# Kernel tuning notes

Hardware: AMD Instinct MI355X
Metric: run time of the kernel (lower is better)

Reference implementation:

```python
import jax, jax.numpy as jnp
import numpy as np

NHEAD = 8; DM = 512; DFF = 2048; L = 4; S = 1024; NTOK = 51; MLP = 256; CLASSES = 7
GH = 3; GHID = 64; GCLS = 5; ALPHA = 0.2
HD = DM // NHEAD

_ADJ = np.array([[0,1,0,0,0],[1,1,1,1,0],[1,0,1,0,1],[1,0,0,1,1],[0,0,1,1,1]], dtype=np.int32)


def setup_inputs():
    key = jax.random.key(0)
    ks = jax.random.split(key, 24)
    r = lambda k, s, sc=0.05: jax.random.normal(k, s, jnp.float32) * sc
    return {
        'x': jax.random.normal(ks[0], (5, S, NTOK), jnp.float32),
        'adj': jnp.asarray(_ADJ),
        'W_enc': r(ks[1], (NTOK, DM)), 'b_enc': jnp.zeros((DM,), jnp.float32),
        'cls_tok': r(ks[2], (1, 1, DM)),
        'pos_emb': r(ks[3], (S + 1, DM)),
        'Wq': r(ks[4], (L, DM, DM)), 'bq': jnp.zeros((L, DM), jnp.float32),
        'Wk': r(ks[5], (L, DM, DM)), 'bk': jnp.zeros((L, DM), jnp.float32),
        'Wv': r(ks[6], (L, DM, DM)), 'bv': jnp.zeros((L, DM), jnp.float32),
        'Wo': r(ks[7], (L, DM, DM)), 'bo': jnp.zeros((L, DM), jnp.float32),
        'W1': r(ks[8], (L, DM, DFF)), 'b1': jnp.zeros((L, DFF), jnp.float32),
        'W2': r(ks[9], (L, DFF, DM)), 'b2': jnp.zeros((L, DM), jnp.float32),
        'g1': jnp.ones((L, DM), jnp.float32), 'be1': jnp.zeros((L, DM), jnp.float32),
        'g2': jnp.ones((L, DM), jnp.float32), 'be2': jnp.zeros((L, DM), jnp.float32),
        'Wd1': r(ks[10], (DM, MLP)), 'bd1': jnp.zeros((MLP,), jnp.float32),
        'Wd2': r(ks[11], (MLP, CLASSES)), 'bd2': jnp.zeros((CLASSES,), jnp.float32),
        'Wg': r(ks[12], (GH, 3, GHID), 0.3), 'ag': r(ks[13], (GH, 2 * GHID), 0.3),
        'Wgo': r(ks[14], (GH * GHID, GCLS), 0.3), 'ago': r(ks[15], (2 * GCLS,), 0.3),
    }


def _layernorm(x, g, b, eps=1e-5):
    m = x.mean(-1, keepdims=True)
    v = ((x - m) ** 2).mean(-1, keepdims=True)
    return (x - m) * jax.lax.rsqrt(v + eps) * g + b


def _gat_attn_layer(h_in, W, a, mask):
    # standard pyGAT GraphAttentionLayer: e_ij = LeakyReLU(a1.h_i + a2.h_j)
    F = W.shape[1]
    h = h_in @ W                                                    # [N, F]
    e = jax.nn.leaky_relu((h @ a[:F])[:, None] + (h @ a[F:])[None, :], ALPHA)
    att = jax.nn.softmax(jnp.where(mask, e, -9e15), axis=-1)        # adjacency-masked softmax
    return att @ h


def _gat(xg, mask, Wg, ag, Wgo, ago):
    # xg: [5 nodes, 3 feats]; GH attention heads concatenated, then output layer
    heads = jax.vmap(lambda W, a: jax.nn.elu(_gat_attn_layer(xg, W, a, mask)))(Wg, ag)  # [GH,5,GHID]
    hcat = jnp.transpose(heads, (1, 0, 2)).reshape(xg.shape[0], GH * GHID)
    out = jax.nn.elu(_gat_attn_layer(hcat, Wgo, ago, mask))         # [5, GCLS]
    return jax.nn.log_softmax(out, axis=1)


def _forward(x, adj, params):
    (W_enc, b_enc, cls_tok, pos_emb, Wq, bq, Wk, bk, Wv, bv, Wo, bo,
     W1, b1, W2, b2, g1, be1, g2, be2, Wd1, bd1, Wd2, bd2, Wg, ag, Wgo, ago) = params
    mask = adj > 0
    # --- batched GAT: the source loops over T timesteps x 5 feature groups; here fully vectorized ---
    # x[:, :, :15] : batch(=5 nodes) x T x 15 -> [T*5groups, 5 nodes, 3]
    xg = x[:, :, :15].reshape(5, S, 5, 3)
    xg = jnp.transpose(xg, (1, 2, 0, 3)).reshape(S * 5, 5, 3)
    gat_out = jax.vmap(lambda g: _gat(g, mask, Wg, ag, Wgo, ago))(xg)
    gat_out = gat_out.reshape(S, 5, 5, GCLS)                        # [T, group, node, class]
    # --- transformer branch (eval mode: dropout = identity) ---
    h = x @ W_enc + b_enc                                           # [5, S, DM]
    h = jnp.concatenate([jnp.broadcast_to(cls_tok, (5, 1, DM)), h], axis=1)
    h = h + pos_emb[None]
    for i in range(L):
        q = (h @ Wq[i] + bq[i]).reshape(5, S + 1, NHEAD, HD)
        k = (h @ Wk[i] + bk[i]).reshape(5, S + 1, NHEAD, HD)
        v = (h @ Wv[i] + bv[i]).reshape(5, S + 1, NHEAD, HD)
        sc = jnp.einsum('bthd,bshd->bhts', q, k) / jnp.sqrt(jnp.float32(HD))
        att = jax.nn.softmax(sc, axis=-1)
        o = jnp.einsum('bhts,bshd->bthd', att, v).reshape(5, S + 1, DM) @ Wo[i] + bo[i]
        h = _layernorm(h + o, g1[i], be1[i])
        f = jax.nn.relu(h @ W1[i] + b1[i]) @ W2[i] + b2[i]
        h = _layernorm(h + f, g2[i], be2[i])
    cls = h[:, 0, :]                                                # lambda: x[:, 0, :]
    out = (cls @ Wd1 + bd1) @ Wd2 + bd2                             # no activation between dense layers (as in source)
    return out, gat_out


def reference(x, adj, W_enc, b_enc, cls_tok, pos_emb, Wq, bq, Wk, bk, Wv, bv, Wo, bo, W1, b1, W2, b2, g1, be1, g2, be2, Wd1, bd1, Wd2, bd2, Wg, ag, Wgo, ago):
    params = (W_enc, b_enc, cls_tok, pos_emb, Wq, bq, Wk, bk, Wv, bv, Wo, bo,
              W1, b1, W2, b2, g1, be1, g2, be2, Wd1, bd1, Wd2, bd2, Wg, ag, Wgo, ago)
    return _forward(x, adj, params)
```

## Files before the change

### kernel.cpp

```cpp
#include <hip/hip_runtime.h>
#include <hip/hip_bf16.h>
#include <math.h>

#define NBATCH 5
#define SEQ    1024
#define T      1025
#define ROWS   (NBATCH * T)
#define MP     5248
#define DM     512
#define DFF    2048
#define NHEAD  8
#define HD     64
#define NTOK   51
#define MLPDIM 256
#define NCLS   7
#define GH     3
#define GHID   64
#define GCLS   5
#define NGRAPH (SEQ * 5)
#define QKVN   1536
#define TPAD   1152

typedef __attribute__((ext_vector_type(8))) short bf16x8;
typedef __attribute__((ext_vector_type(4))) float f32x4;

#define GM_AS(p)  ((const __attribute__((address_space(1))) void*)(p))
#define LDS_AS(p) ((__attribute__((address_space(3))) void*)(p))

__device__ __forceinline__ unsigned short f2bf(float f) {
    unsigned int u = __float_as_uint(f);
    unsigned int r = (u + 0x7FFFu + ((u >> 16) & 1u)) >> 16;
    return (unsigned short)r;
}
__device__ __forceinline__ float bf2f(unsigned short u) {
    return __uint_as_float((unsigned int)u << 16);
}

__global__ __launch_bounds__(256) void setup_kernel(
    const float* __restrict__ Wq, const float* __restrict__ Wk,
    const float* __restrict__ Wv, const float* __restrict__ Wo_,
    const float* __restrict__ W1, const float* __restrict__ W2,
    const float* __restrict__ bq, const float* __restrict__ bk,
    const float* __restrict__ bv,
    unsigned short* __restrict__ Wqkvt, unsigned short* __restrict__ Wot,
    unsigned short* __restrict__ W1t, unsigned short* __restrict__ W2t,
    float* __restrict__ bqkv)
{
    int id = blockIdx.x;
    if (id >= 12288) {
        int i = id - 12288;
        #pragma unroll
        for (int rep = 0; rep < 2; ++rep) {
            int t = threadIdx.x + rep * 256;
            bqkv[i * QKVN + t]        = bq[i * DM + t];
            bqkv[i * QKVN + 512 + t]  = bk[i * DM + t];
            bqkv[i * QKVN + 1024 + t] = bv[i * DM + t];
        }
        return;
    }
    const float* W; unsigned short* Wt; int K, N, z, bx, by; long dstride;
    if (id < 4096) {
        int g = id >> 10, lid = id & 1023;
        K = DM; N = DM;
        z = lid >> 8; int r2 = lid & 255; by = r2 >> 4; bx = r2 & 15;
        if (g < 3) { W = (g == 0) ? Wq : (g == 1) ? Wk : Wv;
                     Wt = Wqkvt + (size_t)g * DM * DM; dstride = (long)QKVN * DM; }
        else       { W = Wo_; Wt = Wot; dstride = (long)DM * DM; }
    } else if (id < 8192) {
        int lid = id - 4096;
        K = DM; N = DFF;
        z = lid >> 10; int r2 = lid & 1023; by = r2 >> 6; bx = r2 & 63;
        W = W1; Wt = W1t; dstride = (long)DM * DFF;
    } else {
        int lid = id - 8192;
        K = DFF; N = DM;
        z = lid >> 10; int r2 = lid & 1023; by = r2 >> 4; bx = r2 & 15;
        W = W2; Wt = W2t; dstride = (long)DFF * DM;
    }
    const float* Wm = W + (size_t)z * K * N;
    unsigned short* Wo2 = Wt + (size_t)z * dstride;
    __shared__ float tile[32][33];
    int bX = bx * 32, bY = by * 32;
    int tx = threadIdx.x & 31, ty = threadIdx.x >> 5;
    #pragma unroll
    for (int i = 0; i < 32; i += 8)
        tile[ty + i][tx] = Wm[(size_t)(bY + ty + i) * N + bX + tx];
    __syncthreads();
    #pragma unroll
    for (int i = 0; i < 32; i += 8)
        Wo2[(size_t)(bX + ty + i) * K + bY + tx] = f2bf(tile[tx][ty + i]);
}

__global__ __launch_bounds__(256) void gemm_mfma(
    const unsigned short* __restrict__ A, const unsigned short* __restrict__ Bt,
    const float* __restrict__ bias, float* __restrict__ Cf,
    unsigned short* __restrict__ Cb, int N, int K, int relu)
{
    __shared__ unsigned short As[128 * 64];
    __shared__ unsigned short Bs[128 * 64];
    int tid = threadIdx.x;
    int l = tid & 63, w = tid >> 6;
    int wr = w & 1, wc = w >> 1;
    int mlane = l & 15, quad = l >> 4;
    int m0 = blockIdx.y * 128, n0 = blockIdx.x * 128;

    f32x4 acc[4][4] = {};

    for (int k0 = 0; k0 < K; k0 += 64) {
        __syncthreads();
        #pragma unroll
        for (int it = 0; it < 4; ++it) {
            int c = tid + it * 256;
            int row = c >> 3, cc = c & 7;
            const unsigned short* ga = A  + (size_t)(m0 + row) * K + k0 + cc * 8;
            __builtin_amdgcn_global_load_lds(GM_AS(ga), LDS_AS(As + c * 8), 16, 0, 0);
            const unsigned short* gb = Bt + (size_t)(n0 + row) * K + k0 + cc * 8;
            __builtin_amdgcn_global_load_lds(GM_AS(gb), LDS_AS(Bs + c * 8), 16, 0, 0);
        }
        __syncthreads();
        #pragma unroll
        for (int half = 0; half < 2; ++half) {
            int ko = half * 32 + quad * 8;
            bf16x8 afrag[4], bfrag[4];
            #pragma unroll
            for (int mi = 0; mi < 4; ++mi)
                afrag[mi] = *(const bf16x8*)(As + (wr * 64 + mi * 16 + mlane) * 64 + ko);
            #pragma unroll
            for (int ni = 0; ni < 4; ++ni)
                bfrag[ni] = *(const bf16x8*)(Bs + (wc * 64 + ni * 16 + mlane) * 64 + ko);
            #pragma unroll
            for (int mi = 0; mi < 4; ++mi)
                #pragma unroll
                for (int ni = 0; ni < 4; ++ni)
                    acc[mi][ni] = __builtin_amdgcn_mfma_f32_16x16x32_bf16(
                        afrag[mi], bfrag[ni], acc[mi][ni], 0, 0, 0);
        }
    }

    #pragma unroll
    for (int mi = 0; mi < 4; ++mi) {
        #pragma unroll
        for (int r = 0; r < 4; ++r) {
            int gm = m0 + wr * 64 + mi * 16 + quad * 4 + r;
            size_t rowoff = (size_t)gm * N;
            #pragma unroll
            for (int ni = 0; ni < 4; ++ni) {
                int gn = n0 + wc * 64 + ni * 16 + mlane;
                float val = acc[mi][ni][r] + bias[gn];
                if (relu) val = fmaxf(val, 0.f);
                if (Cb) Cb[rowoff + gn] = f2bf(val);
                else    Cf[rowoff + gn] = val;
            }
        }
    }
}

__global__ __launch_bounds__(256) void gemm_mfma_sk(
    const unsigned short* __restrict__ A, const unsigned short* __restrict__ Bt,
    unsigned short* __restrict__ part, int N, int K)
{
    __shared__ unsigned short As[128 * 64];
    __shared__ unsigned short Bs[128 * 64];
    int tid = threadIdx.x;
    int l = tid & 63, w = tid >> 6;
    int wr = w & 1, wc = w >> 1;
    int mlane = l & 15, quad = l >> 4;
    int m0 = blockIdx.y * 128, n0 = blockIdx.x * 128;
    int kper = K / gridDim.z;
    int kbeg = blockIdx.z * kper;

    f32x4 acc[4][4] = {};

    for (int k0 = kbeg; k0 < kbeg + kper; k0 += 64) {
        __syncthreads();
        #pragma unroll
        for (int it = 0; it < 4; ++it) {
            int c = tid + it * 256;
            int row = c >> 3, cc = c & 7;
            const unsigned short* ga = A  + (size_t)(m0 + row) * K + k0 + cc * 8;
            __builtin_amdgcn_global_load_lds(GM_AS(ga), LDS_AS(As + c * 8), 16, 0, 0);
            const unsigned short* gb = Bt + (size_t)(n0 + row) * K + k0 + cc * 8;
            __builtin_amdgcn_global_load_lds(GM_AS(gb), LDS_AS(Bs + c * 8), 16, 0, 0);
        }
        __syncthreads();
        #pragma unroll
        for (int half = 0; half < 2; ++half) {
            int ko = half * 32 + quad * 8;
            bf16x8 afrag[4], bfrag[4];
            #pragma unroll
            for (int mi = 0; mi < 4; ++mi)
                afrag[mi] = *(const bf16x8*)(As + (wr * 64 + mi * 16 + mlane) * 64 + ko);
            #pragma unroll
            for (int ni = 0; ni < 4; ++ni)
                bfrag[ni] = *(const bf16x8*)(Bs + (wc * 64 + ni * 16 + mlane) * 64 + ko);
            #pragma unroll
            for (int mi = 0; mi < 4; ++mi)
                #pragma unroll
                for (int ni = 0; ni < 4; ++ni)
                    acc[mi][ni] = __builtin_amdgcn_mfma_f32_16x16x32_bf16(
                        afrag[mi], bfrag[ni], acc[mi][ni], 0, 0, 0);
        }
    }

    unsigned short* pz = part + (size_t)blockIdx.z * MP * N;
    #pragma unroll
    for (int mi = 0; mi < 4; ++mi) {
        #pragma unroll
        for (int r = 0; r < 4; ++r) {
            int gm = m0 + wr * 64 + mi * 16 + quad * 4 + r;
            size_t rowoff = (size_t)gm * N;
            #pragma unroll
            for (int ni = 0; ni < 4; ++ni) {
                int gn = n0 + wc * 64 + ni * 16 + mlane;
                pz[rowoff + gn] = f2bf(acc[mi][ni][r]);
            }
        }
    }
}

__global__ __launch_bounds__(256) void vtrans_kernel(
    const unsigned short* __restrict__ vb, unsigned short* __restrict__ vt, int qs)
{
    __shared__ unsigned short tile[64][72];
    int bh = blockIdx.y;
    int b = bh >> 3, h = bh & 7;
    int t0 = blockIdx.x * 64;
    int tid = threadIdx.x;
    #pragma unroll
    for (int it = 0; it < 2; ++it) {
        int c = tid + it * 256;
        int key = c >> 3, cc = c & 7;
        int gk = t0 + key; if (gk >= T) gk = T - 1;
        *(bf16x8*)(&tile[key][cc * 8]) =
            *(const bf16x8*)(vb + ((size_t)b * T + gk) * qs + h * HD + cc * 8);
    }
    __syncthreads();
    #pragma unroll
    for (int it = 0; it < 2; ++it) {
        int c = tid + it * 256;
        int d = c >> 3, cc = c & 7;
        unsigned short tmp[8];
        #pragma unroll
        for (int j = 0; j < 8; ++j) tmp[j] = tile[cc * 8 + j][d];
        *(bf16x8*)(vt + ((size_t)bh * 64 + d) * TPAD + t0 + cc * 8) = *(bf16x8*)tmp;
    }
}

#define AQT 64
#define NR 9
__global__ __launch_bounds__(256) void attn_mfma(
    const unsigned short* __restrict__ qb, const unsigned short* __restrict__ kb,
    const unsigned short* __restrict__ vt, unsigned short* __restrict__ ob,
    int qs)
{
    __shared__ unsigned short Ks[128 * 72];
    __shared__ unsigned short Vs[64 * 136];
    __shared__ unsigned short Ps[4][16 * 72];
    int bh = blockIdx.y;
    int b = bh >> 3, h = bh & 7;
    int t0 = blockIdx.x * AQT;
    int tid = threadIdx.x;
    int l = tid & 63, w = tid >> 6;
    int ml = l & 15, quad = l >> 4;
    size_t rowbase = (size_t)b * T;
    const unsigned short* vtb = vt + (size_t)bh * 64 * TPAD;

    int qrow = t0 + w * 16 + ml; if (qrow >= T) qrow = T - 1;
    const unsigned short* qp = qb + (rowbase + qrow) * qs + h * HD + quad * 8;
    bf16x8 qf0 = *(const bf16x8*)qp;
    bf16x8 qf1 = *(const bf16x8*)(qp + 32);

    int krow = tid >> 3, kcc = tid & 7;
    int vd   = tid >> 4, vck = tid & 15;

    f32x4 oacc[4] = {};
    float lrow[4] = {0.f, 0.f, 0.f, 0.f};

    bf16x8 kr[4], vr[4];
    #pragma unroll
    for (int i = 0; i < 4; ++i) {
        int gk = krow + i * 32; if (gk >= T) gk = T - 1;
        kr[i] = *(const bf16x8*)(kb + (rowbase + gk) * qs + h * HD + kcc * 8);
        vr[i] = *(const bf16x8*)(vtb + (size_t)(vd + i * 16) * TPAD + vck * 8);
    }

    for (int rnd = 0; rnd < NR; ++rnd) {
        int c0 = rnd * 128;
        __syncthreads();
        #pragma unroll
        for (int i = 0; i < 4; ++i) {
            *(bf16x8*)(Ks + (krow + i * 32) * 72 + kcc * 8) = kr[i];
            *(bf16x8*)(Vs + (vd + i * 16) * 136 + vck * 8) = vr[i];
        }
        __syncthreads();
        if (rnd + 1 < NR) {
            int n0k = c0 + 128;
            #pragma unroll
            for (int i = 0; i < 4; ++i) {
                int gk = n0k + krow + i * 32; if (gk >= T) gk = T - 1;
                kr[i] = *(const bf16x8*)(kb + (rowbase + gk) * qs + h * HD + kcc * 8);
                vr[i] = *(const bf16x8*)(vtb + (size_t)(vd + i * 16) * TPAD + n0k + vck * 8);
            }
        }

        #pragma unroll
        for (int p = 0; p < 2; ++p) {
            int kb0 = p * 64;
            f32x4 s[4] = {};
            #pragma unroll
            for (int ni = 0; ni < 4; ++ni) {
                const unsigned short* kfp = Ks + (kb0 + ni * 16 + ml) * 72 + quad * 8;
                bf16x8 kf0 = *(const bf16x8*)kfp;
                bf16x8 kf1 = *(const bf16x8*)(kfp + 32);
                s[ni] = __builtin_amdgcn_mfma_f32_16x16x32_bf16(qf0, kf0, s[ni], 0, 0, 0);
                s[ni] = __builtin_amdgcn_mfma_f32_16x16x32_bf16(qf1, kf1, s[ni], 0, 0, 0);
            }
            #pragma unroll
            for (int ni = 0; ni < 4; ++ni) {
                bool valid = (c0 + kb0 + ni * 16 + ml) < T;
                #pragma unroll
                for (int r = 0; r < 4; ++r) {
                    float pv = valid ? __expf(s[ni][r] * 0.125f) : 0.f;
                    s[ni][r] = pv;
                    lrow[r] += pv;
                }
            }
            unsigned short* pw = Ps[w];
            #pragma unroll
            for (int r = 0; r < 4; ++r)
                #pragma unroll
                for (int ni = 0; ni < 4; ++ni)
                    pw[(quad * 4 + r) * 72 + ((ni * 16 + ml) ^ (quad << 4))] = f2bf(s[ni][r]);
            int sw = ((ml >> 2) & 3) << 4;
            #pragma unroll
            for (int kc = 0; kc < 2; ++kc) {
                bf16x8 pf = *(const bf16x8*)(pw + ml * 72 + ((kc * 32 + quad * 8) ^ sw));
                #pragma unroll
                for (int ni = 0; ni < 4; ++ni) {
                    bf16x8 vf = *(const bf16x8*)(Vs + (ni * 16 + ml) * 136 + kb0 + kc * 32 + quad * 8);
                    oacc[ni] = __builtin_amdgcn_mfma_f32_16x16x32_bf16(pf, vf, oacc[ni], 0, 0, 0);
                }
            }
        }
    }

    #pragma unroll
    for (int r = 0; r < 4; ++r) {
        #pragma unroll
        for (int off = 1; off < 16; off <<= 1)
            lrow[r] += __shfl_xor(lrow[r], off);
    }
    #pragma unroll
    for (int r = 0; r < 4; ++r) {
        int grow = t0 + w * 16 + quad * 4 + r;
        if (grow >= T) continue;
        float inv = 1.f / lrow[r];
        unsigned short* op = ob + (rowbase + grow) * DM + h * HD;
        #pragma unroll
        for (int ni = 0; ni < 4; ++ni)
            op[ni * 16 + ml] = f2bf(oacc[ni][r] * inv);
    }
}

__global__ __launch_bounds__(256) void encoder_kernel(
    const float* __restrict__ x, const float* __restrict__ W_enc,
    const float* __restrict__ b_enc, const float* __restrict__ cls_tok,
    const float* __restrict__ pos_emb, float* __restrict__ h,
    unsigned short* __restrict__ hb)
{
    int row = blockIdx.x;
    int b = row / T, tt = row % T;
    int tid = threadIdx.x;
    float* hp = h + (size_t)row * DM;
    unsigned short* hbp = hb + (size_t)row * DM;
    if (tt == 0) {
        float a0 = cls_tok[tid]       + pos_emb[tid];
        float a1 = cls_tok[tid + 256] + pos_emb[tid + 256];
        hp[tid] = a0; hp[tid + 256] = a1;
        hbp[tid] = f2bf(a0); hbp[tid + 256] = f2bf(a1);
        return;
    }
    __shared__ float xs[NTOK];
    int s = tt - 1;
    if (tid < NTOK) xs[tid] = x[((size_t)b * SEQ + s) * NTOK + tid];
    __syncthreads();
    #pragma unroll
    for (int rep = 0; rep < 2; ++rep) {
        int d = tid + rep * 256;
        float acc = b_enc[d] + pos_emb[(size_t)tt * DM + d];
        for (int kx = 0; kx < NTOK; ++kx) acc += xs[kx] * W_enc[kx * DM + d];
        hp[d] = acc;
        hbp[d] = f2bf(acc);
    }
}

__global__ __launch_bounds__(256) void add_lnp_kernel(
    float* __restrict__ h, const unsigned short* __restrict__ part, int np,
    const float* __restrict__ bias, const float* __restrict__ g,
    const float* __restrict__ be, unsigned short* __restrict__ hb)
{
    int w = threadIdx.x >> 6, l = threadIdx.x & 63;
    int row = blockIdx.x * 4 + w;
    if (row >= ROWS) return;
    float* hp = h + (size_t)row * DM + l * 8;
    unsigned short* hbp = hb + (size_t)row * DM + l * 8;
    float4 a0 = *(const float4*)(hp);
    float4 a1 = *(const float4*)(hp + 4);
    float4 b0 = *(const float4*)(bias + l * 8);
    float4 b1 = *(const float4*)(bias + l * 8 + 4);
    float v[8] = {a0.x + b0.x, a0.y + b0.y, a0.z + b0.z, a0.w + b0.w,
                  a1.x + b1.x, a1.y + b1.y, a1.z + b1.z, a1.w + b1.w};
    for (int pp = 0; pp < np; ++pp) {
        const unsigned short* prp = part + ((size_t)pp * MP + row) * DM + l * 8;
        bf16x8 pv = *(const bf16x8*)prp;
        #pragma unroll
        for (int i = 0; i < 8; ++i) v[i] += bf2f((unsigned short)pv[i]);
    }
    float s = 0.f;
    #pragma unroll
    for (int i = 0; i < 8; ++i) s += v[i];
    #pragma unroll
    for (int off = 1; off < 64; off <<= 1) s += __shfl_xor(s, off);
    float mean = s * (1.f / DM);
    float sq = 0.f;
    #pragma unroll
    for (int i = 0; i < 8; ++i) { v[i] -= mean; sq += v[i] * v[i]; }
    #pragma unroll
    for (int off = 1; off < 64; off <<= 1) sq += __shfl_xor(sq, off);
    float inv = rsqrtf(sq * (1.f / DM) + 1e-5f);
    float4 g0 = *(const float4*)(g + l * 8);
    float4 g1 = *(const float4*)(g + l * 8 + 4);
    float4 e0 = *(const float4*)(be + l * 8);
    float4 e1 = *(const float4*)(be + l * 8 + 4);
    float o[8];
    o[0] = v[0]*inv*g0.x + e0.x; o[1] = v[1]*inv*g0.y + e0.y;
    o[2] = v[2]*inv*g0.z + e0.z; o[3] = v[3]*inv*g0.w + e0.w;
    o[4] = v[4]*inv*g1.x + e1.x; o[5] = v[5]*inv*g1.y + e1.y;
    o[6] = v[6]*inv*g1.z + e1.z; o[7] = v[7]*inv*g1.w + e1.w;
    *(float4*)(hp)     = make_float4(o[0], o[1], o[2], o[3]);
    *(float4*)(hp + 4) = make_float4(o[4], o[5], o[6], o[7]);
    ushort4 p0 = {f2bf(o[0]), f2bf(o[1]), f2bf(o[2]), f2bf(o[3])};
    ushort4 p1 = {f2bf(o[4]), f2bf(o[5]), f2bf(o[6]), f2bf(o[7])};
    *(ushort4*)(hbp)     = p0;
    *(ushort4*)(hbp + 4) = p1;
}

__global__ __launch_bounds__(256) void dec1_kernel(
    const float* __restrict__ h, const float* __restrict__ Wd1,
    float* __restrict__ part)
{
    int kc = blockIdx.x, b = blockIdx.y, tid = threadIdx.x;
    __shared__ float cs[64];
    const float* cls = h + (size_t)b * T * DM;
    if (tid < 64) cs[tid] = cls[kc * 64 + tid];
    __syncthreads();
    float acc = 0.f;
    #pragma unroll
    for (int kx = 0; kx < 64; ++kx)
        acc += cs[kx] * Wd1[(size_t)(kc * 64 + kx) * MLPDIM + tid];
    part[(size_t)(b * 8 + kc) * MLPDIM + tid] = acc;
}

__global__ __launch_bounds__(256) void dec2_kernel(
    const float* __restrict__ part, const float* __restrict__ bd1,
    const float* __restrict__ Wd2, const float* __restrict__ bd2,
    float* __restrict__ out)
{
    __shared__ float t1s[MLPDIM];
    int tid = threadIdx.x;
    for (int b = 0; b < NBATCH; ++b) {
        float acc = bd1[tid];
        #pragma unroll
        for (int kc = 0; kc < 8; ++kc)
            acc += part[(size_t)(b * 8 + kc) * MLPDIM + tid];
        t1s[tid] = acc;
        __syncthreads();
        if (tid < NCLS) {
            float a2 = bd2[tid];
            for (int kx = 0; kx < MLPDIM; ++kx) a2 += t1s[kx] * Wd2[kx * NCLS + tid];
            out[b * NCLS + tid] = a2;
        }
        __syncthreads();
    }
}

__global__ __launch_bounds__(64) void gat_kernel(
    const float* __restrict__ x, const int* __restrict__ adj,
    const float* __restrict__ Wg, const float* __restrict__ ag,
    const float* __restrict__ Wgo, const float* __restrict__ ago,
    float* __restrict__ out)
{
    int g = blockIdx.x;
    int s = g / 5, jj = g % 5;
    int tid = threadIdx.x;
    __shared__ float xs[5][3];
    __shared__ int adjs[25];
    __shared__ float hb[GH][5][GHID];
    __shared__ float o1[GH][5][GHID];
    __shared__ float srcb[GH][5], dstb[GH][5];
    __shared__ float attb[GH][5][5];
    __shared__ float h2[5][5], src2[5], dst2[5], att2[5][5], o2[5][5];

    if (tid < 15) { int n = tid / 3, c = tid % 3;
        xs[n][c] = x[(size_t)n * SEQ * NTOK + (size_t)s * NTOK + jj * 3 + c]; }
    if (tid < 25) adjs[tid] = adj[tid];
    __syncthreads();

    #pragma unroll
    for (int hh = 0; hh < GH; ++hh)
        #pragma unroll
        for (int n = 0; n < 5; ++n)
            hb[hh][n][tid] = xs[n][0] * Wg[hh * 192 + tid]
                           + xs[n][1] * Wg[hh * 192 + 64 + tid]
                           + xs[n][2] * Wg[hh * 192 + 128 + tid];
    __syncthreads();

    if (tid < 15) { int hh = tid / 5, n = tid % 5; float a = 0.f;
        for (int f = 0; f < GHID; ++f) a += hb[hh][n][f] * ag[hh * 128 + f];
        srcb[hh][n] = a;
    } else if (tid >= 32 && tid < 47) { int t2 = tid - 32; int hh = t2 / 5, n = t2 % 5; float a = 0.f;
        for (int f = 0; f < GHID; ++f) a += hb[hh][n][f] * ag[hh * 128 + 64 + f];
        dstb[hh][n] = a;
    }
    __syncthreads();

    if (tid < 15) { int hh = tid / 5, i = tid % 5;
        float e[5]; float mx = -1e30f;
        #pragma unroll
        for (int j2 = 0; j2 < 5; ++j2) {
            float ev = srcb[hh][i] + dstb[hh][j2];
            ev = ev > 0.f ? ev : 0.2f * ev;
            e[j2] = ev;
            if (adjs[i * 5 + j2] && ev > mx) mx = ev;
        }
        float sum = 0.f;
        #pragma unroll
        for (int j2 = 0; j2 < 5; ++j2) {
            float p = adjs[i * 5 + j2] ? expf(e[j2] - mx) : 0.f;
            e[j2] = p; sum += p;
        }
        float inv = 1.f / sum;
        #pragma unroll
        for (int j2 = 0; j2 < 5; ++j2) attb[hh][i][j2] = e[j2] * inv;
    }
    __syncthreads();

    #pragma unroll
    for (int hh = 0; hh < GH; ++hh)
        #pragma unroll
        for (int n = 0; n < 5; ++n) {
            float a = 0.f;
            #pragma unroll
            for (int j2 = 0; j2 < 5; ++j2) a += attb[hh][n][j2] * hb[hh][j2][tid];
            o1[hh][n][tid] = a > 0.f ? a : expm1f(a);
        }
    __syncthreads();

    if (tid < 25) { int n = tid / 5, m = tid % 5; float a = 0.f;
        for (int hh = 0; hh < GH; ++hh)
            for (int f = 0; f < GHID; ++f)
                a += o1[hh][n][f] * Wgo[(hh * GHID + f) * GCLS + m];
        h2[n][m] = a;
    }
    __syncthreads();

    if (tid < 5) { float a = 0.f;
        for (int m = 0; m < GCLS; ++m) a += h2[tid][m] * ago[m];
        src2[tid] = a;
    } else if (tid >= 8 && tid < 13) { int n = tid - 8; float a = 0.f;
        for (int m = 0; m < GCLS; ++m) a += h2[n][m] * ago[GCLS + m];
        dst2[n] = a;
    }
    __syncthreads();

    if (tid < 5) { int i = tid;
        float e[5]; float mx = -1e30f;
        #pragma unroll
        for (int j2 = 0; j2 < 5; ++j2) {
            float ev = src2[i] + dst2[j2];
            ev = ev > 0.f ? ev : 0.2f * ev;
            e[j2] = ev;
            if (adjs[i * 5 + j2] && ev > mx) mx = ev;
        }
        float sum = 0.f;
        #pragma unroll
        for (int j2 = 0; j2 < 5; ++j2) {
            float p = adjs[i * 5 + j2] ? expf(e[j2] - mx) : 0.f;
            e[j2] = p; sum += p;
        }
        float inv = 1.f / sum;
        #pragma unroll
        for (int j2 = 0; j2 < 5; ++j2) att2[i][j2] = e[j2] * inv;
    }
    __syncthreads();

    if (tid < 25) { int n = tid / 5, m = tid % 5; float a = 0.f;
        #pragma unroll
        for (int j2 = 0; j2 < 5; ++j2) a += att2[n][j2] * h2[j2][m];
        o2[n][m] = a > 0.f ? a : expm1f(a);
    }
    __syncthreads();

    if (tid < 5) { int n = tid;
        float mx = o2[n][0];
        #pragma unroll
        for (int m = 1; m < GCLS; ++m) mx = fmaxf(mx, o2[n][m]);
        float sum = 0.f;
        #pragma unroll
        for (int m = 0; m < GCLS; ++m) sum += expf(o2[n][m] - mx);
        float ls = logf(sum);
        #pragma unroll
        for (int m = 0; m < GCLS; ++m)
            out[(size_t)g * 25 + n * 5 + m] = o2[n][m] - mx - ls;
    }
}

extern "C" void kernel_launch(void* const* d_in, const int* in_sizes, int n_in,
                              void* d_out, int out_size, void* d_ws, size_t ws_size,
                              hipStream_t stream)
{
    const float* x       = (const float*)d_in[0];
    const int*   adj     = (const int*)  d_in[1];
    const float* W_enc   = (const float*)d_in[2];
    const float* b_enc   = (const float*)d_in[3];
    const float* cls_tok = (const float*)d_in[4];
    const float* pos_emb = (const float*)d_in[5];
    const float* Wq = (const float*)d_in[6];
    const float* bq = (const float*)d_in[7];
    const float* Wk = (const float*)d_in[8];
    const float* bk = (const float*)d_in[9];
    const float* Wv = (const float*)d_in[10];
    const float* bv = (const float*)d_in[11];
    const float* Wo = (const float*)d_in[12];
    const float* bo = (const float*)d_in[13];
    const float* W1 = (const float*)d_in[14];
    const float* b1 = (const float*)d_in[15];
    const float* W2 = (const float*)d_in[16];
    const float* b2 = (const float*)d_in[17];
    const float* g1 = (const float*)d_in[18];
    const float* be1= (const float*)d_in[19];
    const float* g2 = (const float*)d_in[20];
    const float* be2= (const float*)d_in[21];
    const float* Wd1= (const float*)d_in[22];
    const float* bd1= (const float*)d_in[23];
    const float* Wd2= (const float*)d_in[24];
    const float* bd2= (const float*)d_in[25];
    const float* Wg = (const float*)d_in[26];
    const float* ag = (const float*)d_in[27];
    const float* Wgo= (const float*)d_in[28];
    const float* ago= (const float*)d_in[29];
    float* out = (float*)d_out;

    float* ws = (float*)d_ws;
    float* h = ws;
    unsigned short* hb   = (unsigned short*)(h + (size_t)MP * DM);
    unsigned short* qkvb = hb + (size_t)MP * DM;
    unsigned short* ob   = qkvb + (size_t)MP * QKVN;
    unsigned short* f1b  = qkvb;
    unsigned short* Wqkvt= ob + (size_t)MP * DM;
    unsigned short* Wot  = Wqkvt + (size_t)4 * QKVN * DM;
    unsigned short* W1t  = Wot + (size_t)4 * DM * DM;
    unsigned short* W2t  = W1t + (size_t)4 * DM * DFF;
    float* bqkv = (float*)(W2t + (size_t)4 * DFF * DM);
    float* dpart = bqkv + 4 * QKVN;
    unsigned short* vt = (unsigned short*)(dpart + NBATCH * 8 * MLPDIM);
    unsigned short* parts = vt + (size_t)40 * 64 * TPAD;

    setup_kernel<<<12292, 256, 0, stream>>>(Wq, Wk, Wv, Wo, W1, W2, bq, bk, bv,
                                            Wqkvt, Wot, W1t, W2t, bqkv);

    gat_kernel<<<NGRAPH, 64, 0, stream>>>(x, adj, Wg, ag, Wgo, ago, out + NBATCH * NCLS);
    encoder_kernel<<<ROWS, 256, 0, stream>>>(x, W_enc, b_enc, cls_tok, pos_emb, h, hb);

    dim3 gqkv (QKVN / 128, MP / 128);
    dim3 g2048(DFF / 128, MP / 128);
    dim3 gWo  (DM / 128, MP / 128, 2);
    dim3 gW2  (DM / 128, MP / 128, 4);
    dim3 gAttn(17, NBATCH * NHEAD);
    dim3 gVt  (TPAD / 64, NBATCH * NHEAD);
    int gLN = (ROWS + 3) / 4;

    for (int i = 0; i < 4; ++i) {
        gemm_mfma<<<gqkv, 256, 0, stream>>>(hb, Wqkvt + (size_t)i*QKVN*DM, bqkv + i*QKVN, nullptr, qkvb, QKVN, DM, 0);
        vtrans_kernel<<<gVt, 256, 0, stream>>>(qkvb + 1024, vt, QKVN);
        attn_mfma<<<gAttn, 256, 0, stream>>>(qkvb, qkvb + 512, vt, ob, QKVN);
        gemm_mfma_sk<<<gWo, 256, 0, stream>>>(ob, Wot + (size_t)i*DM*DM, parts, DM, DM);
        add_lnp_kernel<<<gLN, 256, 0, stream>>>(h, parts, 2, bo + i*DM, g1 + i*DM, be1 + i*DM, hb);
        gemm_mfma<<<g2048, 256, 0, stream>>>(hb,  W1t + (size_t)i*DM*DFF, b1 + i*DFF, nullptr, f1b, DFF, DM, 1);
        gemm_mfma_sk<<<gW2, 256, 0, stream>>>(f1b, W2t + (size_t)i*DM*DFF, parts, DM, DFF);
        add_lnp_kernel<<<gLN, 256, 0, stream>>>(h, parts, 4, b2 + i*DM, g2 + i*DM, be2 + i*DM, hb);
    }

    dec1_kernel<<<dim3(8, NBATCH), 256, 0, stream>>>(h, Wd1, dpart);
    dec2_kernel<<<1, 256, 0, stream>>>(dpart, bd1, Wd2, bd2, out);
}
```

Measured before the change: 798.8 us.

## Fuse V transpose into QKV GEMM epilogue and pack four GAT graphs per block

The QKV GEMM epilogue now also writes the V columns (n >= 1024) straight into the transposed per-head vt buffer, using packed 4-element stores along t. This removes the separate vtrans kernel launch and its extra read and write of V in each of the four layers. The GAT kernel now handles four graphs per 256-thread block, one wavefront each, so the launch uses a quarter as many small blocks. In exchange, the GEMM epilogue does strided and often unaligned scattered stores, because T is odd. The padded tail of vt beyond T is also no longer written, so it may hold stale data.

```diff
diff --git a/kernel.cpp b/kernel.cpp
--- a/kernel.cpp
+++ b/kernel.cpp
@@ -94,7 +94,8 @@
 __global__ __launch_bounds__(256) void gemm_mfma(
     const unsigned short* __restrict__ A, const unsigned short* __restrict__ Bt,
     const float* __restrict__ bias, float* __restrict__ Cf,
-    unsigned short* __restrict__ Cb, int N, int K, int relu)
+    unsigned short* __restrict__ Cb, unsigned short* __restrict__ vt,
+    int N, int K, int relu)
 {
     __shared__ unsigned short As[128 * 64];
     __shared__ unsigned short Bs[128 * 64];
@@ -150,6 +151,41 @@
                 if (relu) val = fmaxf(val, 0.f);
                 if (Cb) Cb[rowoff + gn] = f2bf(val);
                 else    Cf[rowoff + gn] = val;
+            }
+        }
+    }
+
+    if (vt && n0 + wc * 64 >= 1024) {
+        #pragma unroll
+        for (int mi = 0; mi < 4; ++mi) {
+            int gm0 = m0 + wr * 64 + mi * 16 + quad * 4;
+            if (gm0 >= ROWS) continue;
+            int b = gm0 / T;
+            int t = gm0 - b * T;
+            bool pack = (t + 3 < T) && (gm0 + 3 < ROWS);
+            #pragma unroll
+            for (int ni = 0; ni < 4; ++ni) {
+                int gn = n0 + wc * 64 + ni * 16 + mlane;
+                int hd = gn - 1024;
+                float bs = bias[gn];
+                if (pack) {
+                    int bh = b * 8 + (hd >> 6), d = hd & 63;
+                    ushort4 pk;
+                    pk.x = f2bf(acc[mi][ni][0] + bs);
+                    pk.y = f2bf(acc[mi][ni][1] + bs);
+                    pk.z = f2bf(acc[mi][ni][2] + bs);
+                    pk.w = f2bf(acc[mi][ni][3] + bs);
+                    *(ushort4*)(vt + (size_t)(bh * 64 + d) * TPAD + t) = pk;
+                } else {
+                    #pragma unroll
+                    for (int r = 0; r < 4; ++r) {
+                        int gmr = gm0 + r;
+                        if (gmr >= ROWS) continue;
+                        int br = gmr / T, tr = gmr - br * T;
+                        int bh = br * 8 + (hd >> 6), d = hd & 63;
+                        vt[(size_t)(bh * 64 + d) * TPAD + tr] = f2bf(acc[mi][ni][r] + bs);
+                    }
+                }
             }
         }
     }
@@ -215,34 +251,6 @@
                 pz[rowoff + gn] = f2bf(acc[mi][ni][r]);
             }
         }
-    }
-}
-
-__global__ __launch_bounds__(256) void vtrans_kernel(
-    const unsigned short* __restrict__ vb, unsigned short* __restrict__ vt, int qs)
-{
-    __shared__ unsigned short tile[64][72];
-    int bh = blockIdx.y;
-    int b = bh >> 3, h = bh & 7;
-    int t0 = blockIdx.x * 64;
-    int tid = threadIdx.x;
-    #pragma unroll
-    for (int it = 0; it < 2; ++it) {
-        int c = tid + it * 256;
-        int key = c >> 3, cc = c & 7;
-        int gk = t0 + key; if (gk >= T) gk = T - 1;
-        *(bf16x8*)(&tile[key][cc * 8]) =
-            *(const bf16x8*)(vb + ((size_t)b * T + gk) * qs + h * HD + cc * 8);
-    }
-    __syncthreads();
-    #pragma unroll
-    for (int it = 0; it < 2; ++it) {
-        int c = tid + it * 256;
-        int d = c >> 3, cc = c & 7;
-        unsigned short tmp[8];
-        #pragma unroll
-        for (int j = 0; j < 8; ++j) tmp[j] = tile[cc * 8 + j][d];
-        *(bf16x8*)(vt + ((size_t)bh * 64 + d) * TPAD + t0 + cc * 8) = *(bf16x8*)tmp;
     }
 }
 
@@ -484,43 +492,44 @@
     }
 }
 
-__global__ __launch_bounds__(64) void gat_kernel(
+__global__ __launch_bounds__(256) void gat_kernel(
     const float* __restrict__ x, const int* __restrict__ adj,
     const float* __restrict__ Wg, const float* __restrict__ ag,
     const float* __restrict__ Wgo, const float* __restrict__ ago,
     float* __restrict__ out)
 {
-    int g = blockIdx.x;
+    int w4 = threadIdx.x >> 6;
+    int tid = threadIdx.x & 63;
+    int g = blockIdx.x * 4 + w4;
     int s = g / 5, jj = g % 5;
-    int tid = threadIdx.x;
-    __shared__ float xs[5][3];
-    __shared__ int adjs[25];
-    __shared__ float hb[GH][5][GHID];
-    __shared__ float o1[GH][5][GHID];
-    __shared__ float srcb[GH][5], dstb[GH][5];
-    __shared__ float attb[GH][5][5];
-    __shared__ float h2[5][5], src2[5], dst2[5], att2[5][5], o2[5][5];
+    __shared__ float xs[4][5][3];
+    __shared__ int adjs[4][25];
+    __shared__ float hb[4][GH][5][GHID];
+    __shared__ float o1[4][GH][5][GHID];
+    __shared__ float srcb[4][GH][5], dstb[4][GH][5];
+    __shared__ float attb[4][GH][5][5];
+    __shared__ float h2[4][5][5], src2[4][5], dst2[4][5], att2[4][5][5], o2[4][5][5];
 
     if (tid < 15) { int n = tid / 3, c = tid % 3;
-        xs[n][c] = x[(size_t)n * SEQ * NTOK + (size_t)s * NTOK + jj * 3 + c]; }
-    if (tid < 25) adjs[tid] = adj[tid];
+        xs[w4][n][c] = x[(size_t)n * SEQ * NTOK + (size_t)s * NTOK + jj * 3 + c]; }
+    if (tid < 25) adjs[w4][tid] = adj[tid];
     __syncthreads();
 
     #pragma unroll
     for (int hh = 0; hh < GH; ++hh)
         #pragma unroll
         for (int n = 0; n < 5; ++n)
-            hb[hh][n][tid] = xs[n][0] * Wg[hh * 192 + tid]
-                           + xs[n][1] * Wg[hh * 192 + 64 + tid]
-                           + xs[n][2] * Wg[hh * 192 + 128 + tid];
+            hb[w4][hh][n][tid] = xs[w4][n][0] * Wg[hh * 192 + tid]
+                               + xs[w4][n][1] * Wg[hh * 192 + 64 + tid]
+                               + xs[w4][n][2] * Wg[hh * 192 + 128 + tid];
     __syncthreads();
 
     if (tid < 15) { int hh = tid / 5, n = tid % 5; float a = 0.f;
-        for (int f = 0; f < GHID; ++f) a += hb[hh][n][f] * ag[hh * 128 + f];
-        srcb[hh][n] = a;
+        for (int f = 0; f < GHID; ++f) a += hb[w4][hh][n][f] * ag[hh * 128 + f];
+        srcb[w4][hh][n] = a;
     } else if (tid >= 32 && tid < 47) { int t2 = tid - 32; int hh = t2 / 5, n = t2 % 5; float a = 0.f;
-        for (int f = 0; f < GHID; ++f) a += hb[hh][n][f] * ag[hh * 128 + 64 + f];
-        dstb[hh][n] = a;
+        for (int f = 0; f < GHID; ++f) a += hb[w4][hh][n][f] * ag[hh * 128 + 64 + f];
+        dstb[w4][hh][n] = a;
     }
     __syncthreads();
 
@@ -528,20 +537,20 @@
         float e[5]; float mx = -1e30f;
         #pragma unroll
         for (int j2 = 0; j2 < 5; ++j2) {
-            float ev = srcb[hh][i] + dstb[hh][j2];
+            float ev = srcb[w4][hh][i] + dstb[w4][hh][j2];
             ev = ev > 0.f ? ev : 0.2f * ev;
             e[j2] = ev;
-            if (adjs[i * 5 + j2] && ev > mx) mx = ev;
+            if (adjs[w4][i * 5 + j2] && ev > mx) mx = ev;
         }
         float sum = 0.f;
         #pragma unroll
         for (int j2 = 0; j2 < 5; ++j2) {
-            float p = adjs[i * 5 + j2] ? expf(e[j2] - mx) : 0.f;
+            float p = adjs[w4][i * 5 + j2] ? expf(e[j2] - mx) : 0.f;
             e[j2] = p; sum += p;
         }
         float inv = 1.f / sum;
         #pragma unroll
-        for (int j2 = 0; j2 < 5; ++j2) attb[hh][i][j2] = e[j2] * inv;
+        for (int j2 = 0; j2 < 5; ++j2) attb[w4][hh][i][j2] = e[j2] * inv;
     }
     __syncthreads();
 
@@ -551,25 +560,25 @@
         for (int n = 0; n < 5; ++n) {
             float a = 0.f;
             #pragma unroll
-            for (int j2 = 0; j2 < 5; ++j2) a += attb[hh][n][j2] * hb[hh][j2][tid];
-            o1[hh][n][tid] = a > 0.f ? a : expm1f(a);
+            for (int j2 = 0; j2 < 5; ++j2) a += attb[w4][hh][n][j2] * hb[w4][hh][j2][tid];
+            o1[w4][hh][n][tid] = a > 0.f ? a : expm1f(a);
         }
     __syncthreads();
 
     if (tid < 25) { int n = tid / 5, m = tid % 5; float a = 0.f;
         for (int hh = 0; hh < GH; ++hh)
             for (int f = 0; f < GHID; ++f)
-                a += o1[hh][n][f] * Wgo[(hh * GHID + f) * GCLS + m];
-        h2[n][m] = a;
+                a += o1[w4][hh][n][f] * Wgo[(hh * GHID + f) * GCLS + m];
+        h2[w4][n][m] = a;
     }
     __syncthreads();
 
     if (tid < 5) { float a = 0.f;
-        for (int m = 0; m < GCLS; ++m) a += h2[tid][m] * ago[m];
-        src2[tid] = a;
+        for (int m = 0; m < GCLS; ++m) a += h2[w4][tid][m] * ago[m];
+        src2[w4][tid] = a;
     } else if (tid >= 8 && tid < 13) { int n = tid - 8; float a = 0.f;
-        for (int m = 0; m < GCLS; ++m) a += h2[n][m] * ago[GCLS + m];
-        dst2[n] = a;
+        for (int m = 0; m < GCLS; ++m) a += h2[w4][n][m] * ago[GCLS + m];
+        dst2[w4][n] = a;
     }
     __syncthreads();
 
@@ -577,41 +586,41 @@
         float e[5]; float mx = -1e30f;
         #pragma unroll
         for (int j2 = 0; j2 < 5; ++j2) {
-            float ev = src2[i] + dst2[j2];
+            float ev = src2[w4][i] + dst2[w4][j2];
             ev = ev > 0.f ? ev : 0.2f * ev;
             e[j2] = ev;
-            if (adjs[i * 5 + j2] && ev > mx) mx = ev;
+            if (adjs[w4][i * 5 + j2] && ev > mx) mx = ev;
         }
         float sum = 0.f;
         #pragma unroll
         for (int j2 = 0; j2 < 5; ++j2) {
-            float p = adjs[i * 5 + j2] ? expf(e[j2] - mx) : 0.f;
+            float p = adjs[w4][i * 5 + j2] ? expf(e[j2] - mx) : 0.f;
             e[j2] = p; sum += p;
         }
         float inv = 1.f / sum;
         #pragma unroll
-        for (int j2 = 0; j2 < 5; ++j2) att2[i][j2] = e[j2] * inv;
+        for (int j2 = 0; j2 < 5; ++j2) att2[w4][i][j2] = e[j2] * inv;
     }
     __syncthreads();
 
     if (tid < 25) { int n = tid / 5, m = tid % 5; float a = 0.f;
         #pragma unroll
-        for (int j2 = 0; j2 < 5; ++j2) a += att2[n][j2] * h2[j2][m];
-        o2[n][m] = a > 0.f ? a : expm1f(a);
+        for (int j2 = 0; j2 < 5; ++j2) a += att2[w4][n][j2] * h2[w4][j2][m];
+        o2[w4][n][m] = a > 0.f ? a : expm1f(a);
     }
     __syncthreads();
 
     if (tid < 5) { int n = tid;
-        float mx = o2[n][0];
-        #pragma unroll
-        for (int m = 1; m < GCLS; ++m) mx = fmaxf(mx, o2[n][m]);
+        float mx = o2[w4][n][0];
+        #pragma unroll
+        for (int m = 1; m < GCLS; ++m) mx = fmaxf(mx, o2[w4][n][m]);
         float sum = 0.f;
         #pragma unroll
-        for (int m = 0; m < GCLS; ++m) sum += expf(o2[n][m] - mx);
+        for (int m = 0; m < GCLS; ++m) sum += expf(o2[w4][n][m] - mx);
         float ls = logf(sum);
         #pragma unroll
         for (int m = 0; m < GCLS; ++m)
-            out[(size_t)g * 25 + n * 5 + m] = o2[n][m] - mx - ls;
+            out[(size_t)g * 25 + n * 5 + m] = o2[w4][n][m] - mx - ls;
     }
 }
 
@@ -669,7 +678,7 @@
     setup_kernel<<<12292, 256, 0, stream>>>(Wq, Wk, Wv, Wo, W1, W2, bq, bk, bv,
                                             Wqkvt, Wot, W1t, W2t, bqkv);
 
-    gat_kernel<<<NGRAPH, 64, 0, stream>>>(x, adj, Wg, ag, Wgo, ago, out + NBATCH * NCLS);
+    gat_kernel<<<NGRAPH / 4, 256, 0, stream>>>(x, adj, Wg, ag, Wgo, ago, out + NBATCH * NCLS);
     encoder_kernel<<<ROWS, 256, 0, stream>>>(x, W_enc, b_enc, cls_tok, pos_emb, h, hb);
 
     dim3 gqkv (QKVN / 128, MP / 128);
@@ -677,16 +686,14 @@
     dim3 gWo  (DM / 128, MP / 128, 2);
     dim3 gW2  (DM / 128, MP / 128, 4);
     dim3 gAttn(17, NBATCH * NHEAD);
-    dim3 gVt  (TPAD / 64, NBATCH * NHEAD);
     int gLN = (ROWS + 3) / 4;
 
     for (int i = 0; i < 4; ++i) {
-        gemm_mfma<<<gqkv, 256, 0, stream>>>(hb, Wqkvt + (size_t)i*QKVN*DM, bqkv + i*QKVN, nullptr, qkvb, QKVN, DM, 0);
-        vtrans_kernel<<<gVt, 256, 0, stream>>>(qkvb + 1024, vt, QKVN);
+        gemm_mfma<<<gqkv, 256, 0, stream>>>(hb, Wqkvt + (size_t)i*QKVN*DM, bqkv + i*QKVN, nullptr, qkvb, vt, QKVN, DM, 0);
         attn_mfma<<<gAttn, 256, 0, stream>>>(qkvb, qkvb + 512, vt, ob, QKVN);
         gemm_mfma_sk<<<gWo, 256, 0, stream>>>(ob, Wot + (size_t)i*DM*DM, parts, DM, DM);
         add_lnp_kernel<<<gLN, 256, 0, stream>>>(h, parts, 2, bo + i*DM, g1 + i*DM, be1 + i*DM, hb);
-        gemm_mfma<<<g2048, 256, 0, stream>>>(hb,  W1t + (size_t)i*DM*DFF, b1 + i*DFF, nullptr, f1b, DFF, DM, 1);
+        gemm_mfma<<<g2048, 256, 0, stream>>>(hb,  W1t + (size_t)i*DM*DFF, b1 + i*DFF, nullptr, f1b, nullptr, DFF, DM, 1);
         gemm_mfma_sk<<<gW2, 256, 0, stream>>>(f1b, W2t + (size_t)i*DM*DFF, parts, DM, DFF);
         add_lnp_kernel<<<gLN, 256, 0, stream>>>(h, parts, 4, b2 + i*DM, g2 + i*DM, be2 + i*DM, hb);
     }
```

Measured after the change: 829.0 us. 3.8% more time.
